# Performance work log

Measured on AMD Instinct MI355X. Metric: run time of the kernel, lower is better.

The kernel has to match this reference:

```python
import jax, jax.numpy as jnp
import numpy as np

B, T, D = 2048, 200, 64
H1, H2 = 80, 40
NEG_INF = -4294967295.0  # -(2**32) + 1 as in original


def setup_inputs() -> dict:
    key0 = jax.random.key(0)
    ks = jax.random.split(key0, 10)
    din_dim = 4 * D
    inp = {
        "query": jax.random.normal(ks[0], (B, D), dtype=jnp.float32),
        "key": jax.random.normal(ks[1], (B, T, D), dtype=jnp.float32),
        "mask": jax.random.randint(ks[2], (B,), 1, T + 1, dtype=jnp.int32),
        # MLP params (Dense 4D->80->40->1, use_bias=True)
        "W1": jax.random.normal(ks[3], (din_dim, H1), dtype=jnp.float32) / np.sqrt(din_dim),
        "b1": jnp.zeros((H1,), dtype=jnp.float32),
        "W2": jax.random.normal(ks[4], (H1, H2), dtype=jnp.float32) / np.sqrt(H1),
        "b2": jnp.zeros((H2,), dtype=jnp.float32),
        "W3": jax.random.normal(ks[5], (H2, 1), dtype=jnp.float32) / np.sqrt(H2),
        "b3": jnp.zeros((1,), dtype=jnp.float32),
    }
    return inp


def reference(query, key, mask, W1, b1, W2, b2, W3, b3):
    b, t, d = key.shape
    q = query[:, None, :]                      # [B,1,D]
    q_tile = jnp.broadcast_to(q, (b, t, d))    # [B,T,D]
    din_all = jnp.concatenate([q_tile, key, q_tile - key, q_tile * key], axis=-1)  # [B,T,4D]
    h = jax.nn.sigmoid(jnp.einsum("btf,fh->bth", din_all, W1) + b1)
    h = jax.nn.sigmoid(jnp.einsum("bth,hg->btg", h, W2) + b2)
    score = (jnp.einsum("btg,go->bto", h, W3) + b3)[..., 0]  # [B,T]
    key_mask = jnp.arange(t)[None, :] < mask[:, None]        # [B,T]
    score = jnp.where(key_mask, score, NEG_INF)
    score = score / jnp.asarray(d, score.dtype) ** 0.5
    attn = jax.nn.softmax(score, axis=-1)                    # [B,T]
    out = jnp.einsum("bt,btd->bd", attn, key)                # [B,D] (squeezed)
    return out
```

## Files before the change

kernel.cpp:

```cpp
#include <hip/hip_runtime.h>
#include <math.h>

#define B_  2048
#define T_  200
#define D_  64
#define H1_ 80
#define H2_ 40

#define VSTR 72
#define WSTR 104
#define HSTR 104

#define WS_A    0
#define WS_C    10240
#define WS_W2T  20480
#define WS_ACT  30464

typedef __bf16 bf16x8 __attribute__((ext_vector_type(8)));
typedef float  f32x4  __attribute__((ext_vector_type(4)));

__device__ __forceinline__ float sigmoidf_(float x) {
    return __builtin_amdgcn_rcpf(1.0f + __expf(-x));
}

__global__ __launch_bounds__(256)
void prep_kernel(const float* __restrict__ W1, const float* __restrict__ W2,
                 void* __restrict__ ws)
{
    __bf16* A    = (__bf16*)((char*)ws + WS_A);
    __bf16* C    = (__bf16*)((char*)ws + WS_C);
    __bf16* W2Tp = (__bf16*)((char*)ws + WS_W2T);
    float*  acT  = (float*)((char*)ws + WS_ACT);
    const int e0 = blockIdx.x * 256 + threadIdx.x;

    for (int e = e0; e < H1_ * D_; e += 2048) {
        int h = e >> 6, f = e & 63;
        float wb = W1[(64  + f) * H1_ + h];
        float wc = W1[(128 + f) * H1_ + h];
        float wd = W1[(192 + f) * H1_ + h];
        float wa = W1[f * H1_ + h];
        A[e]   = (__bf16)(wb - wc);
        C[e]   = (__bf16)wd;
        acT[e] = wa + wc;
    }
    for (int e = e0; e < 48 * WSTR; e += 2048) {
        int g = e / WSTR, h = e - g * WSTR;
        W2Tp[e] = (g < H2_ && h < H1_) ? (__bf16)W2[h * H2_ + g] : (__bf16)0.0f;
    }
}

__global__ __launch_bounds__(256, 2)
void attn_din9(const float* __restrict__ query,
               const float* __restrict__ key,
               const int*   __restrict__ mask,
               const float* __restrict__ b1,
               const float* __restrict__ b2,
               const float* __restrict__ W3,
               const float* __restrict__ b3,
               const void*  __restrict__ ws,
               float* __restrict__ out)
{
    __shared__ __align__(16) __bf16 s_V[4][H1_ * VSTR];
    __shared__ __align__(16) __bf16 s_h1[4][16 * HSTR];
    __shared__ float  s_scf[4][208];
    __shared__ float  s_q[4][D_];
    __shared__ float  s_base[4][H1_];

    const int tid  = threadIdx.x;
    const int lane = tid & 63;
    const int w    = tid >> 6;
    const int c16  = lane & 15;
    const int g16  = lane >> 4;
    const int b    = blockIdx.x * 4 + w;

    const int   mv     = mask[b];
    const int   ntiles = (mv + 15) >> 4;
    const float b3v    = b3[0];
    const float* kb = key + (size_t)b * T_ * D_;

    const __bf16* wsA   = (const __bf16*)((const char*)ws + WS_A);
    const __bf16* wsC   = (const __bf16*)((const char*)ws + WS_C);
    const __bf16* wsW2T = (const __bf16*)((const char*)ws + WS_W2T);
    const float*  wsacT = (const float*) ((const char*)ws + WS_ACT);

    float qv = query[b * D_ + lane];
    float4 u0, u1, u2, u3;
    {
        int tr = c16;
        const float* kr = kb + (size_t)tr * D_ + g16 * 8;
        u0 = *(const float4*)(kr);
        u1 = *(const float4*)(kr + 4);
        u2 = *(const float4*)(kr + 32);
        u3 = *(const float4*)(kr + 36);
    }

    s_scf[w][lane]       = -1e30f;
    s_scf[w][64 + lane]  = -1e30f;
    s_scf[w][128 + lane] = -1e30f;
    if (lane < 16) s_scf[w][192 + lane] = -1e30f;

    bf16x8 bw[3][3];
    #pragma unroll
    for (int nt = 0; nt < 3; ++nt)
        #pragma unroll
        for (int ks = 0; ks < 3; ++ks)
            bw[nt][ks] = *(const bf16x8*)&wsW2T[(nt * 16 + c16) * WSTR + ks * 32 + g16 * 8];

    float b2c[3], w3c[3];
    #pragma unroll
    for (int nt = 0; nt < 3; ++nt) {
        int g = nt * 16 + c16;
        b2c[nt] = (g < H2_) ? b2[g] : 0.0f;
        w3c[nt] = (g < H2_) ? W3[g] : 0.0f;
    }

    s_q[w][lane] = qv;

    #pragma unroll
    for (int i = 0; i < 10; ++i) {
        int e = lane + 64 * i;
        int h = e >> 3, f8 = e & 7;
        bf16x8 a8 = *(const bf16x8*)&wsA[e * 8];
        bf16x8 c8 = *(const bf16x8*)&wsC[e * 8];
        f32x4 q0 = *(const f32x4*)&s_q[w][f8 * 8];
        f32x4 q1 = *(const f32x4*)&s_q[w][f8 * 8 + 4];
        bf16x8 v8;
        v8[0] = (__bf16)((float)a8[0] + q0[0] * (float)c8[0]);
        v8[1] = (__bf16)((float)a8[1] + q0[1] * (float)c8[1]);
        v8[2] = (__bf16)((float)a8[2] + q0[2] * (float)c8[2]);
        v8[3] = (__bf16)((float)a8[3] + q0[3] * (float)c8[3]);
        v8[4] = (__bf16)((float)a8[4] + q1[0] * (float)c8[4]);
        v8[5] = (__bf16)((float)a8[5] + q1[1] * (float)c8[5]);
        v8[6] = (__bf16)((float)a8[6] + q1[2] * (float)c8[6]);
        v8[7] = (__bf16)((float)a8[7] + q1[3] * (float)c8[7]);
        *(bf16x8*)&s_V[w][h * VSTR + f8 * 8] = v8;
    }

    {
        float a0 = b1[lane], a1 = 0.0f, a2 = 0.0f, a3 = 0.0f;
        const f32x4* row = (const f32x4*)&wsacT[lane * D_];
        #pragma unroll
        for (int f4 = 0; f4 < 16; ++f4) {
            f32x4 v  = row[f4];
            f32x4 q4 = *(const f32x4*)&s_q[w][f4 * 4];
            a0 = fmaf(q4[0], v[0], a0);
            a1 = fmaf(q4[1], v[1], a1);
            a2 = fmaf(q4[2], v[2], a2);
            a3 = fmaf(q4[3], v[3], a3);
        }
        s_base[w][lane] = (a0 + a1) + (a2 + a3);
    }
    if (lane < 16) {
        int h = 64 + lane;
        float a0 = b1[h], a1 = 0.0f, a2 = 0.0f, a3 = 0.0f;
        const f32x4* row = (const f32x4*)&wsacT[h * D_];
        #pragma unroll
        for (int f4 = 0; f4 < 16; ++f4) {
            f32x4 v  = row[f4];
            f32x4 q4 = *(const f32x4*)&s_q[w][f4 * 4];
            a0 = fmaf(q4[0], v[0], a0);
            a1 = fmaf(q4[1], v[1], a1);
            a2 = fmaf(q4[2], v[2], a2);
            a3 = fmaf(q4[3], v[3], a3);
        }
        s_base[w][h] = (a0 + a1) + (a2 + a3);
    }

    {
        int row = lane & 15, c0 = 80 + (lane >> 4) * 4;
        *(uint2*)&s_h1[w][row * HSTR + c0] = make_uint2(0u, 0u);
    }

    float base_c[5];
    #pragma unroll
    for (int nt = 0; nt < 5; ++nt) base_c[nt] = s_base[w][nt * 16 + c16];
    __bf16* myh = &s_h1[w][0];

    for (int tt = 0; tt < ntiles; ++tt) {
        bf16x8 af0, af1;
        af0[0] = (__bf16)u0.x; af0[1] = (__bf16)u0.y; af0[2] = (__bf16)u0.z; af0[3] = (__bf16)u0.w;
        af0[4] = (__bf16)u1.x; af0[5] = (__bf16)u1.y; af0[6] = (__bf16)u1.z; af0[7] = (__bf16)u1.w;
        af1[0] = (__bf16)u2.x; af1[1] = (__bf16)u2.y; af1[2] = (__bf16)u2.z; af1[3] = (__bf16)u2.w;
        af1[4] = (__bf16)u3.x; af1[5] = (__bf16)u3.y; af1[6] = (__bf16)u3.z; af1[7] = (__bf16)u3.w;

        if (tt + 1 < ntiles) {
            int tr = (tt + 1) * 16 + c16;
            const float* kr = kb + (size_t)((tr < T_) ? tr : (T_ - 1)) * D_ + g16 * 8;
            u0 = *(const float4*)(kr);
            u1 = *(const float4*)(kr + 4);
            u2 = *(const float4*)(kr + 32);
            u3 = *(const float4*)(kr + 36);
        }

        #pragma unroll
        for (int nt = 0; nt < 5; ++nt) {
            float bb = base_c[nt];
            f32x4 c = { bb, bb, bb, bb };
            bf16x8 bv0 = *(const bf16x8*)&s_V[w][(nt * 16 + c16) * VSTR + g16 * 8];
            bf16x8 bv1 = *(const bf16x8*)&s_V[w][(nt * 16 + c16) * VSTR + 32 + g16 * 8];
            c = __builtin_amdgcn_mfma_f32_16x16x32_bf16(af0, bv0, c, 0, 0, 0);
            c = __builtin_amdgcn_mfma_f32_16x16x32_bf16(af1, bv1, c, 0, 0, 0);
            #pragma unroll
            for (int r = 0; r < 4; ++r)
                myh[(g16 * 4 + r) * HSTR + nt * 16 + c16] = (__bf16)sigmoidf_(c[r]);
        }

        bf16x8 a2_0 = *(const bf16x8*)&myh[c16 * HSTR + g16 * 8];
        bf16x8 a2_1 = *(const bf16x8*)&myh[c16 * HSTR + 32 + g16 * 8];
        bf16x8 a2_2 = *(const bf16x8*)&myh[c16 * HSTR + 64 + g16 * 8];
        f32x4 acc2[3];
        #pragma unroll
        for (int nt = 0; nt < 3; ++nt) {
            float bb = b2c[nt];
            f32x4 c = { bb, bb, bb, bb };
            c = __builtin_amdgcn_mfma_f32_16x16x32_bf16(a2_0, bw[nt][0], c, 0, 0, 0);
            c = __builtin_amdgcn_mfma_f32_16x16x32_bf16(a2_1, bw[nt][1], c, 0, 0, 0);
            c = __builtin_amdgcn_mfma_f32_16x16x32_bf16(a2_2, bw[nt][2], c, 0, 0, 0);
            acc2[nt] = c;
        }

        const int tb = tt * 16;
        #pragma unroll
        for (int r = 0; r < 4; ++r) {
            float partial = sigmoidf_(acc2[0][r]) * w3c[0]
                          + sigmoidf_(acc2[1][r]) * w3c[1]
                          + sigmoidf_(acc2[2][r]) * w3c[2];
            partial += __shfl_xor(partial, 1);
            partial += __shfl_xor(partial, 2);
            partial += __shfl_xor(partial, 4);
            partial += __shfl_xor(partial, 8);
            int t = tb + g16 * 4 + r;
            if (c16 == 0 && t < mv)
                s_scf[w][t] = (partial + b3v) * 0.125f;
        }
    }
    asm volatile("s_waitcnt lgkmcnt(0)" ::: "memory");

    float s0 = s_scf[w][lane];
    float s1 = s_scf[w][64 + lane];
    float s2 = s_scf[w][128 + lane];
    float s3 = (lane < 16) ? s_scf[w][192 + lane] : -1e30f;
    float m = fmaxf(fmaxf(s0, s1), fmaxf(s2, s3));
    #pragma unroll
    for (int off = 32; off >= 1; off >>= 1) m = fmaxf(m, __shfl_xor(m, off));
    float p0 = __expf(s0 - m), p1 = __expf(s1 - m);
    float p2 = __expf(s2 - m), p3 = (lane < 16) ? __expf(s3 - m) : 0.0f;
    float ps = (p0 + p1) + (p2 + p3);
    #pragma unroll
    for (int off = 32; off >= 1; off >>= 1) ps += __shfl_xor(ps, off);
    float inv_total = __builtin_amdgcn_rcpf(ps);
    s_scf[w][lane]       = p0;
    s_scf[w][64 + lane]  = p1;
    s_scf[w][128 + lane] = p2;
    if (lane < 16) s_scf[w][192 + lane] = p3;
    asm volatile("s_waitcnt lgkmcnt(0)" ::: "memory");

    float a0 = 0.0f, a1 = 0.0f, a2s = 0.0f, a3s = 0.0f;
    const float* ksc = &s_scf[w][0];
    int t = 0;
    for (; t + 4 <= mv; t += 4) {
        a0  = fmaf(ksc[t],     kb[(t)     * D_ + lane], a0);
        a1  = fmaf(ksc[t + 1], kb[(t + 1) * D_ + lane], a1);
        a2s = fmaf(ksc[t + 2], kb[(t + 2) * D_ + lane], a2s);
        a3s = fmaf(ksc[t + 3], kb[(t + 3) * D_ + lane], a3s);
    }
    for (; t < mv; ++t)
        a0 = fmaf(ksc[t], kb[t * D_ + lane], a0);
    out[b * D_ + lane] = ((a0 + a1) + (a2s + a3s)) * inv_total;
}

extern "C" void kernel_launch(void* const* d_in, const int* in_sizes, int n_in,
                              void* d_out, int out_size, void* d_ws, size_t ws_size,
                              hipStream_t stream)
{
    const float* query = (const float*)d_in[0];
    const float* key   = (const float*)d_in[1];
    const int*   mask  = (const int*)  d_in[2];
    const float* W1    = (const float*)d_in[3];
    const float* b1    = (const float*)d_in[4];
    const float* W2    = (const float*)d_in[5];
    const float* b2    = (const float*)d_in[6];
    const float* W3    = (const float*)d_in[7];
    const float* b3    = (const float*)d_in[8];
    float* out = (float*)d_out;

    prep_kernel<<<8, 256, 0, stream>>>(W1, W2, d_ws);
    attn_din9<<<512, 256, 0, stream>>>(query, key, mask, b1, b2, W3, b3, d_ws, out);
}
```

Before: 47.49 us.

## Fuse online softmax and weighted key sum into MLP tile loop; keep V in registers

Replaces the post-loop softmax and second pass over the key rows with an online (flash-style) softmax. The loop rescales running max, sum and per-lane output accumulators each 16-row tile, using the key values already loaded for the MFMA A operand. This removes the second global read of key and the score buffer in shared memory. The per-batch first-layer weight matrix V is now built directly in registers as MFMA B fragments instead of staged through LDS. The cost is higher register pressure (extra accumulators plus 10 bf16x8 fragments) and per-tile shuffle reductions.

Result: slower. 49.18 us (+3.6%).

```diff
diff --git a/kernel.cpp b/kernel.cpp
--- a/kernel.cpp
+++ b/kernel.cpp
@@ -7,7 +7,6 @@
 #define H1_ 80
 #define H2_ 40
 
-#define VSTR 72
 #define WSTR 104
 #define HSTR 104
 
@@ -50,21 +49,21 @@
 }
 
 __global__ __launch_bounds__(256, 2)
-void attn_din9(const float* __restrict__ query,
-               const float* __restrict__ key,
-               const int*   __restrict__ mask,
-               const float* __restrict__ b1,
-               const float* __restrict__ b2,
-               const float* __restrict__ W3,
-               const float* __restrict__ b3,
-               const void*  __restrict__ ws,
-               float* __restrict__ out)
+void attn_din10(const float* __restrict__ query,
+                const float* __restrict__ key,
+                const int*   __restrict__ mask,
+                const float* __restrict__ b1,
+                const float* __restrict__ b2,
+                const float* __restrict__ W3,
+                const float* __restrict__ b3,
+                const void*  __restrict__ ws,
+                float* __restrict__ out)
 {
-    __shared__ __align__(16) __bf16 s_V[4][H1_ * VSTR];
     __shared__ __align__(16) __bf16 s_h1[4][16 * HSTR];
-    __shared__ float  s_scf[4][208];
-    __shared__ float  s_q[4][D_];
-    __shared__ float  s_base[4][H1_];
+    __shared__ __align__(16) float  s_q[4][D_];
+    __shared__ float s_base[4][H1_];
+    __shared__ float s_sc16[4][16];
+    __shared__ float s_part[4][D_];
 
     const int tid  = threadIdx.x;
     const int lane = tid & 63;
@@ -86,18 +85,13 @@
     float qv = query[b * D_ + lane];
     float4 u0, u1, u2, u3;
     {
-        int tr = c16;
-        const float* kr = kb + (size_t)tr * D_ + g16 * 8;
+        const float* kr = kb + (size_t)c16 * D_ + g16 * 8;
         u0 = *(const float4*)(kr);
         u1 = *(const float4*)(kr + 4);
         u2 = *(const float4*)(kr + 32);
         u3 = *(const float4*)(kr + 36);
     }
-
-    s_scf[w][lane]       = -1e30f;
-    s_scf[w][64 + lane]  = -1e30f;
-    s_scf[w][128 + lane] = -1e30f;
-    if (lane < 16) s_scf[w][192 + lane] = -1e30f;
+    s_q[w][lane] = qv;
 
     bf16x8 bw[3][3];
     #pragma unroll
@@ -112,28 +106,6 @@
         int g = nt * 16 + c16;
         b2c[nt] = (g < H2_) ? b2[g] : 0.0f;
         w3c[nt] = (g < H2_) ? W3[g] : 0.0f;
-    }
-
-    s_q[w][lane] = qv;
-
-    #pragma unroll
-    for (int i = 0; i < 10; ++i) {
-        int e = lane + 64 * i;
-        int h = e >> 3, f8 = e & 7;
-        bf16x8 a8 = *(const bf16x8*)&wsA[e * 8];
-        bf16x8 c8 = *(const bf16x8*)&wsC[e * 8];
-        f32x4 q0 = *(const f32x4*)&s_q[w][f8 * 8];
-        f32x4 q1 = *(const f32x4*)&s_q[w][f8 * 8 + 4];
-        bf16x8 v8;
-        v8[0] = (__bf16)((float)a8[0] + q0[0] * (float)c8[0]);
-        v8[1] = (__bf16)((float)a8[1] + q0[1] * (float)c8[1]);
-        v8[2] = (__bf16)((float)a8[2] + q0[2] * (float)c8[2]);
-        v8[3] = (__bf16)((float)a8[3] + q0[3] * (float)c8[3]);
-        v8[4] = (__bf16)((float)a8[4] + q1[0] * (float)c8[4]);
-        v8[5] = (__bf16)((float)a8[5] + q1[1] * (float)c8[5]);
-        v8[6] = (__bf16)((float)a8[6] + q1[2] * (float)c8[6]);
-        v8[7] = (__bf16)((float)a8[7] + q1[3] * (float)c8[7]);
-        *(bf16x8*)&s_V[w][h * VSTR + f8 * 8] = v8;
     }
 
     {
@@ -166,6 +138,28 @@
         s_base[w][h] = (a0 + a1) + (a2 + a3);
     }
 
+    bf16x8 bv[5][2];
+    #pragma unroll
+    for (int nt = 0; nt < 5; ++nt)
+        #pragma unroll
+        for (int ks = 0; ks < 2; ++ks) {
+            int off = (nt * 16 + c16) * D_ + ks * 32 + g16 * 8;
+            bf16x8 a8 = *(const bf16x8*)&wsA[off];
+            bf16x8 c8 = *(const bf16x8*)&wsC[off];
+            f32x4 q0 = *(const f32x4*)&s_q[w][ks * 32 + g16 * 8];
+            f32x4 q1 = *(const f32x4*)&s_q[w][ks * 32 + g16 * 8 + 4];
+            bf16x8 v8;
+            v8[0] = (__bf16)((float)a8[0] + q0[0] * (float)c8[0]);
+            v8[1] = (__bf16)((float)a8[1] + q0[1] * (float)c8[1]);
+            v8[2] = (__bf16)((float)a8[2] + q0[2] * (float)c8[2]);
+            v8[3] = (__bf16)((float)a8[3] + q0[3] * (float)c8[3]);
+            v8[4] = (__bf16)((float)a8[4] + q1[0] * (float)c8[4]);
+            v8[5] = (__bf16)((float)a8[5] + q1[1] * (float)c8[5]);
+            v8[6] = (__bf16)((float)a8[6] + q1[2] * (float)c8[6]);
+            v8[7] = (__bf16)((float)a8[7] + q1[3] * (float)c8[7]);
+            bv[nt][ks] = v8;
+        }
+
     {
         int row = lane & 15, c0 = 80 + (lane >> 4) * 4;
         *(uint2*)&s_h1[w][row * HSTR + c0] = make_uint2(0u, 0u);
@@ -175,6 +169,10 @@
     #pragma unroll
     for (int nt = 0; nt < 5; ++nt) base_c[nt] = s_base[w][nt * 16 + c16];
     __bf16* myh = &s_h1[w][0];
+
+    float o00,o01,o02,o03,o04,o05,o06,o07,o08,o09,o10,o11,o12,o13,o14,o15;
+    o00=o01=o02=o03=o04=o05=o06=o07=o08=o09=o10=o11=o12=o13=o14=o15=0.0f;
+    float m_run = -1e30f, l_run = 0.0f;
 
     for (int tt = 0; tt < ntiles; ++tt) {
         bf16x8 af0, af1;
@@ -183,23 +181,22 @@
         af1[0] = (__bf16)u2.x; af1[1] = (__bf16)u2.y; af1[2] = (__bf16)u2.z; af1[3] = (__bf16)u2.w;
         af1[4] = (__bf16)u3.x; af1[5] = (__bf16)u3.y; af1[6] = (__bf16)u3.z; af1[7] = (__bf16)u3.w;
 
+        float4 n0 = u0, n1 = u1, n2 = u2, n3 = u3;
         if (tt + 1 < ntiles) {
             int tr = (tt + 1) * 16 + c16;
             const float* kr = kb + (size_t)((tr < T_) ? tr : (T_ - 1)) * D_ + g16 * 8;
-            u0 = *(const float4*)(kr);
-            u1 = *(const float4*)(kr + 4);
-            u2 = *(const float4*)(kr + 32);
-            u3 = *(const float4*)(kr + 36);
+            n0 = *(const float4*)(kr);
+            n1 = *(const float4*)(kr + 4);
+            n2 = *(const float4*)(kr + 32);
+            n3 = *(const float4*)(kr + 36);
         }
 
         #pragma unroll
         for (int nt = 0; nt < 5; ++nt) {
             float bb = base_c[nt];
             f32x4 c = { bb, bb, bb, bb };
-            bf16x8 bv0 = *(const bf16x8*)&s_V[w][(nt * 16 + c16) * VSTR + g16 * 8];
-            bf16x8 bv1 = *(const bf16x8*)&s_V[w][(nt * 16 + c16) * VSTR + 32 + g16 * 8];
-            c = __builtin_amdgcn_mfma_f32_16x16x32_bf16(af0, bv0, c, 0, 0, 0);
-            c = __builtin_amdgcn_mfma_f32_16x16x32_bf16(af1, bv1, c, 0, 0, 0);
+            c = __builtin_amdgcn_mfma_f32_16x16x32_bf16(af0, bv[nt][0], c, 0, 0, 0);
+            c = __builtin_amdgcn_mfma_f32_16x16x32_bf16(af1, bv[nt][1], c, 0, 0, 0);
             #pragma unroll
             for (int r = 0; r < 4; ++r)
                 myh[(g16 * 4 + r) * HSTR + nt * 16 + c16] = (__bf16)sigmoidf_(c[r]);
@@ -229,44 +226,58 @@
             partial += __shfl_xor(partial, 2);
             partial += __shfl_xor(partial, 4);
             partial += __shfl_xor(partial, 8);
-            int t = tb + g16 * 4 + r;
-            if (c16 == 0 && t < mv)
-                s_scf[w][t] = (partial + b3v) * 0.125f;
-        }
+            if (c16 == 0) {
+                int t = tb + g16 * 4 + r;
+                s_sc16[w][g16 * 4 + r] = (t < mv) ? (partial + b3v) * 0.125f : -1e30f;
+            }
+        }
+
+        float s = s_sc16[w][c16];
+        float tm = s;
+        tm = fmaxf(tm, __shfl_xor(tm, 1));
+        tm = fmaxf(tm, __shfl_xor(tm, 2));
+        tm = fmaxf(tm, __shfl_xor(tm, 4));
+        tm = fmaxf(tm, __shfl_xor(tm, 8));
+        float m_new = fmaxf(m_run, tm);
+        float alpha = __expf(m_run - m_new);
+        float p = __expf(s - m_new);
+        float psum = p;
+        psum += __shfl_xor(psum, 1);
+        psum += __shfl_xor(psum, 2);
+        psum += __shfl_xor(psum, 4);
+        psum += __shfl_xor(psum, 8);
+        l_run = l_run * alpha + psum;
+        o00 = o00 * alpha + p * u0.x;  o01 = o01 * alpha + p * u0.y;
+        o02 = o02 * alpha + p * u0.z;  o03 = o03 * alpha + p * u0.w;
+        o04 = o04 * alpha + p * u1.x;  o05 = o05 * alpha + p * u1.y;
+        o06 = o06 * alpha + p * u1.z;  o07 = o07 * alpha + p * u1.w;
+        o08 = o08 * alpha + p * u2.x;  o09 = o09 * alpha + p * u2.y;
+        o10 = o10 * alpha + p * u2.z;  o11 = o11 * alpha + p * u2.w;
+        o12 = o12 * alpha + p * u3.x;  o13 = o13 * alpha + p * u3.y;
+        o14 = o14 * alpha + p * u3.z;  o15 = o15 * alpha + p * u3.w;
+        m_run = m_new;
+
+        u0 = n0; u1 = n1; u2 = n2; u3 = n3;
+    }
+
+    #define ORED(X) X += __shfl_xor(X,1); X += __shfl_xor(X,2); X += __shfl_xor(X,4); X += __shfl_xor(X,8);
+    ORED(o00) ORED(o01) ORED(o02) ORED(o03) ORED(o04) ORED(o05) ORED(o06) ORED(o07)
+    ORED(o08) ORED(o09) ORED(o10) ORED(o11) ORED(o12) ORED(o13) ORED(o14) ORED(o15)
+    #undef ORED
+    float inv_total = __builtin_amdgcn_rcpf(l_run);
+    if (c16 == 0) {
+        float* sp = &s_part[w][0];
+        sp[g16 * 8 + 0] = o00;  sp[g16 * 8 + 1] = o01;
+        sp[g16 * 8 + 2] = o02;  sp[g16 * 8 + 3] = o03;
+        sp[g16 * 8 + 4] = o04;  sp[g16 * 8 + 5] = o05;
+        sp[g16 * 8 + 6] = o06;  sp[g16 * 8 + 7] = o07;
+        sp[32 + g16 * 8 + 0] = o08;  sp[32 + g16 * 8 + 1] = o09;
+        sp[32 + g16 * 8 + 2] = o10;  sp[32 + g16 * 8 + 3] = o11;
+        sp[32 + g16 * 8 + 4] = o12;  sp[32 + g16 * 8 + 5] = o13;
+        sp[32 + g16 * 8 + 6] = o14;  sp[32 + g16 * 8 + 7] = o15;
     }
     asm volatile("s_waitcnt lgkmcnt(0)" ::: "memory");
-
-    float s0 = s_scf[w][lane];
-    float s1 = s_scf[w][64 + lane];
-    float s2 = s_scf[w][128 + lane];
-    float s3 = (lane < 16) ? s_scf[w][192 + lane] : -1e30f;
-    float m = fmaxf(fmaxf(s0, s1), fmaxf(s2, s3));
-    #pragma unroll
-    for (int off = 32; off >= 1; off >>= 1) m = fmaxf(m, __shfl_xor(m, off));
-    float p0 = __expf(s0 - m), p1 = __expf(s1 - m);
-    float p2 = __expf(s2 - m), p3 = (lane < 16) ? __expf(s3 - m) : 0.0f;
-    float ps = (p0 + p1) + (p2 + p3);
-    #pragma unroll
-    for (int off = 32; off >= 1; off >>= 1) ps += __shfl_xor(ps, off);
-    float inv_total = __builtin_amdgcn_rcpf(ps);
-    s_scf[w][lane]       = p0;
-    s_scf[w][64 + lane]  = p1;
-    s_scf[w][128 + lane] = p2;
-    if (lane < 16) s_scf[w][192 + lane] = p3;
-    asm volatile("s_waitcnt lgkmcnt(0)" ::: "memory");
-
-    float a0 = 0.0f, a1 = 0.0f, a2s = 0.0f, a3s = 0.0f;
-    const float* ksc = &s_scf[w][0];
-    int t = 0;
-    for (; t + 4 <= mv; t += 4) {
-        a0  = fmaf(ksc[t],     kb[(t)     * D_ + lane], a0);
-        a1  = fmaf(ksc[t + 1], kb[(t + 1) * D_ + lane], a1);
-        a2s = fmaf(ksc[t + 2], kb[(t + 2) * D_ + lane], a2s);
-        a3s = fmaf(ksc[t + 3], kb[(t + 3) * D_ + lane], a3s);
-    }
-    for (; t < mv; ++t)
-        a0 = fmaf(ksc[t], kb[t * D_ + lane], a0);
-    out[b * D_ + lane] = ((a0 + a1) + (a2s + a3s)) * inv_total;
+    out[b * D_ + lane] = s_part[w][lane] * inv_total;
 }
 
 extern "C" void kernel_launch(void* const* d_in, const int* in_sizes, int n_in,
@@ -285,5 +296,5 @@
     float* out = (float*)d_out;
 
     prep_kernel<<<8, 256, 0, stream>>>(W1, W2, d_ws);
-    attn_din9<<<512, 256, 0, stream>>>(query, key, mask, b1, b2, W3, b3, d_ws, out);
+    attn_din10<<<512, 256, 0, stream>>>(query, key, mask, b1, b2, W3, b3, d_ws, out);
 }
```

## Split each batch row across two waves instead of one wave per row

Applied to the files above, without the earlier changes.

Each block now handles a single batch row with two waves. The waves interleave the 16-row key tiles and share one s_V/s_base table that is built cooperatively. Softmax max/sum and the final weighted sum are combined across the two waves through shared memory and __syncthreads. This is meant to fix load imbalance from variable mask lengths and halve per-row latency, at the cost of extra block barriers and 2048 smaller blocks.

After: 51.63 us. +8.7%, slower.

```diff
diff --git a/kernel.cpp b/kernel.cpp
--- a/kernel.cpp
+++ b/kernel.cpp
@@ -49,29 +49,31 @@
     }
 }
 
-__global__ __launch_bounds__(256, 2)
-void attn_din9(const float* __restrict__ query,
-               const float* __restrict__ key,
-               const int*   __restrict__ mask,
-               const float* __restrict__ b1,
-               const float* __restrict__ b2,
-               const float* __restrict__ W3,
-               const float* __restrict__ b3,
-               const void*  __restrict__ ws,
-               float* __restrict__ out)
+__global__ __launch_bounds__(128, 3)
+void attn_din12(const float* __restrict__ query,
+                const float* __restrict__ key,
+                const int*   __restrict__ mask,
+                const float* __restrict__ b1,
+                const float* __restrict__ b2,
+                const float* __restrict__ W3,
+                const float* __restrict__ b3,
+                const void*  __restrict__ ws,
+                float* __restrict__ out)
 {
-    __shared__ __align__(16) __bf16 s_V[4][H1_ * VSTR];
-    __shared__ __align__(16) __bf16 s_h1[4][16 * HSTR];
-    __shared__ float  s_scf[4][208];
-    __shared__ float  s_q[4][D_];
-    __shared__ float  s_base[4][H1_];
+    __shared__ __align__(16) __bf16 s_V[H1_ * VSTR];
+    __shared__ __align__(16) __bf16 s_h1[2][16 * HSTR];
+    __shared__ float s_scf[208];
+    __shared__ float s_q[D_];
+    __shared__ float s_base[H1_];
+    __shared__ float s_part[2][D_];
+    __shared__ float s_red[4];
 
     const int tid  = threadIdx.x;
     const int lane = tid & 63;
     const int w    = tid >> 6;
     const int c16  = lane & 15;
     const int g16  = lane >> 4;
-    const int b    = blockIdx.x * 4 + w;
+    const int b    = blockIdx.x;
 
     const int   mv     = mask[b];
     const int   ntiles = (mv + 15) >> 4;
@@ -83,21 +85,8 @@
     const __bf16* wsW2T = (const __bf16*)((const char*)ws + WS_W2T);
     const float*  wsacT = (const float*) ((const char*)ws + WS_ACT);
 
-    float qv = query[b * D_ + lane];
-    float4 u0, u1, u2, u3;
-    {
-        int tr = c16;
-        const float* kr = kb + (size_t)tr * D_ + g16 * 8;
-        u0 = *(const float4*)(kr);
-        u1 = *(const float4*)(kr + 4);
-        u2 = *(const float4*)(kr + 32);
-        u3 = *(const float4*)(kr + 36);
-    }
-
-    s_scf[w][lane]       = -1e30f;
-    s_scf[w][64 + lane]  = -1e30f;
-    s_scf[w][128 + lane] = -1e30f;
-    if (lane < 16) s_scf[w][192 + lane] = -1e30f;
+    if (w == 0) s_q[lane] = query[b * D_ + lane];
+    for (int i = tid; i < 208; i += 128) s_scf[i] = -1e30f;
 
     bf16x8 bw[3][3];
     #pragma unroll
@@ -113,17 +102,16 @@
         b2c[nt] = (g < H2_) ? b2[g] : 0.0f;
         w3c[nt] = (g < H2_) ? W3[g] : 0.0f;
     }
-
-    s_q[w][lane] = qv;
-
-    #pragma unroll
-    for (int i = 0; i < 10; ++i) {
-        int e = lane + 64 * i;
+    __syncthreads();
+
+    #pragma unroll
+    for (int i = 0; i < 5; ++i) {
+        int e = tid + 128 * i;
         int h = e >> 3, f8 = e & 7;
         bf16x8 a8 = *(const bf16x8*)&wsA[e * 8];
         bf16x8 c8 = *(const bf16x8*)&wsC[e * 8];
-        f32x4 q0 = *(const f32x4*)&s_q[w][f8 * 8];
-        f32x4 q1 = *(const f32x4*)&s_q[w][f8 * 8 + 4];
+        f32x4 q0 = *(const f32x4*)&s_q[f8 * 8];
+        f32x4 q1 = *(const f32x4*)&s_q[f8 * 8 + 4];
         bf16x8 v8;
         v8[0] = (__bf16)((float)a8[0] + q0[0] * (float)c8[0]);
         v8[1] = (__bf16)((float)a8[1] + q0[1] * (float)c8[1]);
@@ -133,58 +121,54 @@
         v8[5] = (__bf16)((float)a8[5] + q1[1] * (float)c8[5]);
         v8[6] = (__bf16)((float)a8[6] + q1[2] * (float)c8[6]);
         v8[7] = (__bf16)((float)a8[7] + q1[3] * (float)c8[7]);
-        *(bf16x8*)&s_V[w][h * VSTR + f8 * 8] = v8;
-    }
-
-    {
-        float a0 = b1[lane], a1 = 0.0f, a2 = 0.0f, a3 = 0.0f;
-        const f32x4* row = (const f32x4*)&wsacT[lane * D_];
+        *(bf16x8*)&s_V[h * VSTR + f8 * 8] = v8;
+    }
+
+    if (tid < H1_) {
+        float a0 = b1[tid], a1 = 0.0f, a2 = 0.0f, a3 = 0.0f;
+        const f32x4* row = (const f32x4*)&wsacT[tid * D_];
         #pragma unroll
         for (int f4 = 0; f4 < 16; ++f4) {
             f32x4 v  = row[f4];
-            f32x4 q4 = *(const f32x4*)&s_q[w][f4 * 4];
+            f32x4 q4 = *(const f32x4*)&s_q[f4 * 4];
             a0 = fmaf(q4[0], v[0], a0);
             a1 = fmaf(q4[1], v[1], a1);
             a2 = fmaf(q4[2], v[2], a2);
             a3 = fmaf(q4[3], v[3], a3);
         }
-        s_base[w][lane] = (a0 + a1) + (a2 + a3);
-    }
-    if (lane < 16) {
-        int h = 64 + lane;
-        float a0 = b1[h], a1 = 0.0f, a2 = 0.0f, a3 = 0.0f;
-        const f32x4* row = (const f32x4*)&wsacT[h * D_];
-        #pragma unroll
-        for (int f4 = 0; f4 < 16; ++f4) {
-            f32x4 v  = row[f4];
-            f32x4 q4 = *(const f32x4*)&s_q[w][f4 * 4];
-            a0 = fmaf(q4[0], v[0], a0);
-            a1 = fmaf(q4[1], v[1], a1);
-            a2 = fmaf(q4[2], v[2], a2);
-            a3 = fmaf(q4[3], v[3], a3);
-        }
-        s_base[w][h] = (a0 + a1) + (a2 + a3);
+        s_base[tid] = (a0 + a1) + (a2 + a3);
     }
 
     {
         int row = lane & 15, c0 = 80 + (lane >> 4) * 4;
         *(uint2*)&s_h1[w][row * HSTR + c0] = make_uint2(0u, 0u);
     }
+    __syncthreads();
 
     float base_c[5];
     #pragma unroll
-    for (int nt = 0; nt < 5; ++nt) base_c[nt] = s_base[w][nt * 16 + c16];
+    for (int nt = 0; nt < 5; ++nt) base_c[nt] = s_base[nt * 16 + c16];
     __bf16* myh = &s_h1[w][0];
 
-    for (int tt = 0; tt < ntiles; ++tt) {
+    float4 u0, u1, u2, u3;
+    {
+        int tr = w * 16 + c16;
+        const float* kr = kb + (size_t)((tr < T_) ? tr : (T_ - 1)) * D_ + g16 * 8;
+        u0 = *(const float4*)(kr);
+        u1 = *(const float4*)(kr + 4);
+        u2 = *(const float4*)(kr + 32);
+        u3 = *(const float4*)(kr + 36);
+    }
+
+    for (int tt = w; tt < ntiles; tt += 2) {
         bf16x8 af0, af1;
         af0[0] = (__bf16)u0.x; af0[1] = (__bf16)u0.y; af0[2] = (__bf16)u0.z; af0[3] = (__bf16)u0.w;
         af0[4] = (__bf16)u1.x; af0[5] = (__bf16)u1.y; af0[6] = (__bf16)u1.z; af0[7] = (__bf16)u1.w;
         af1[0] = (__bf16)u2.x; af1[1] = (__bf16)u2.y; af1[2] = (__bf16)u2.z; af1[3] = (__bf16)u2.w;
         af1[4] = (__bf16)u3.x; af1[5] = (__bf16)u3.y; af1[6] = (__bf16)u3.z; af1[7] = (__bf16)u3.w;
 
-        if (tt + 1 < ntiles) {
-            int tr = (tt + 1) * 16 + c16;
+        if (tt + 2 < ntiles) {
+            int tr = (tt + 2) * 16 + c16;
             const float* kr = kb + (size_t)((tr < T_) ? tr : (T_ - 1)) * D_ + g16 * 8;
             u0 = *(const float4*)(kr);
             u1 = *(const float4*)(kr + 4);
@@ -196,8 +180,8 @@
         for (int nt = 0; nt < 5; ++nt) {
             float bb = base_c[nt];
             f32x4 c = { bb, bb, bb, bb };
-            bf16x8 bv0 = *(const bf16x8*)&s_V[w][(nt * 16 + c16) * VSTR + g16 * 8];
-            bf16x8 bv1 = *(const bf16x8*)&s_V[w][(nt * 16 + c16) * VSTR + 32 + g16 * 8];
+            bf16x8 bv0 = *(const bf16x8*)&s_V[(nt * 16 + c16) * VSTR + g16 * 8];
+            bf16x8 bv1 = *(const bf16x8*)&s_V[(nt * 16 + c16) * VSTR + 32 + g16 * 8];
             c = __builtin_amdgcn_mfma_f32_16x16x32_bf16(af0, bv0, c, 0, 0, 0);
             c = __builtin_amdgcn_mfma_f32_16x16x32_bf16(af1, bv1, c, 0, 0, 0);
             #pragma unroll
@@ -231,42 +215,49 @@
             partial += __shfl_xor(partial, 8);
             int t = tb + g16 * 4 + r;
             if (c16 == 0 && t < mv)
-                s_scf[w][t] = (partial + b3v) * 0.125f;
-        }
-    }
-    asm volatile("s_waitcnt lgkmcnt(0)" ::: "memory");
-
-    float s0 = s_scf[w][lane];
-    float s1 = s_scf[w][64 + lane];
-    float s2 = s_scf[w][128 + lane];
-    float s3 = (lane < 16) ? s_scf[w][192 + lane] : -1e30f;
-    float m = fmaxf(fmaxf(s0, s1), fmaxf(s2, s3));
+                s_scf[t] = (partial + b3v) * 0.125f;
+        }
+    }
+    __syncthreads();
+
+    float s0 = s_scf[tid];
+    float s1 = (tid + 128 < 208) ? s_scf[tid + 128] : -1e30f;
+    float m = fmaxf(s0, s1);
     #pragma unroll
     for (int off = 32; off >= 1; off >>= 1) m = fmaxf(m, __shfl_xor(m, off));
-    float p0 = __expf(s0 - m), p1 = __expf(s1 - m);
-    float p2 = __expf(s2 - m), p3 = (lane < 16) ? __expf(s3 - m) : 0.0f;
-    float ps = (p0 + p1) + (p2 + p3);
+    if (lane == 0) s_red[w] = m;
+    __syncthreads();
+    m = fmaxf(s_red[0], s_red[1]);
+    float p0 = __expf(s0 - m);
+    float p1 = (tid + 128 < 208) ? __expf(s1 - m) : 0.0f;
+    float ps = p0 + p1;
     #pragma unroll
     for (int off = 32; off >= 1; off >>= 1) ps += __shfl_xor(ps, off);
-    float inv_total = __builtin_amdgcn_rcpf(ps);
-    s_scf[w][lane]       = p0;
-    s_scf[w][64 + lane]  = p1;
-    s_scf[w][128 + lane] = p2;
-    if (lane < 16) s_scf[w][192 + lane] = p3;
-    asm volatile("s_waitcnt lgkmcnt(0)" ::: "memory");
+    if (lane == 0) s_red[2 + w] = ps;
+    __syncthreads();
+    float inv_total = __builtin_amdgcn_rcpf(s_red[2] + s_red[3]);
+    s_scf[tid] = p0;
+    if (tid + 128 < 208) s_scf[tid + 128] = p1;
+    __syncthreads();
 
     float a0 = 0.0f, a1 = 0.0f, a2s = 0.0f, a3s = 0.0f;
-    const float* ksc = &s_scf[w][0];
-    int t = 0;
-    for (; t + 4 <= mv; t += 4) {
-        a0  = fmaf(ksc[t],     kb[(t)     * D_ + lane], a0);
-        a1  = fmaf(ksc[t + 1], kb[(t + 1) * D_ + lane], a1);
-        a2s = fmaf(ksc[t + 2], kb[(t + 2) * D_ + lane], a2s);
-        a3s = fmaf(ksc[t + 3], kb[(t + 3) * D_ + lane], a3s);
-    }
-    for (; t < mv; ++t)
-        a0 = fmaf(ksc[t], kb[t * D_ + lane], a0);
-    out[b * D_ + lane] = ((a0 + a1) + (a2s + a3s)) * inv_total;
+    for (int tt = w; tt < ntiles; tt += 2) {
+        int t0 = tt * 16;
+        int tend = (t0 + 16 < mv) ? (t0 + 16) : mv;
+        int t = t0;
+        for (; t + 4 <= tend; t += 4) {
+            a0  = fmaf(s_scf[t],     kb[(t)     * D_ + lane], a0);
+            a1  = fmaf(s_scf[t + 1], kb[(t + 1) * D_ + lane], a1);
+            a2s = fmaf(s_scf[t + 2], kb[(t + 2) * D_ + lane], a2s);
+            a3s = fmaf(s_scf[t + 3], kb[(t + 3) * D_ + lane], a3s);
+        }
+        for (; t < tend; ++t)
+            a0 = fmaf(s_scf[t], kb[t * D_ + lane], a0);
+    }
+    s_part[w][lane] = (a0 + a1) + (a2s + a3s);
+    __syncthreads();
+    if (tid < D_)
+        out[b * D_ + tid] = (s_part[0][tid] + s_part[1][tid]) * inv_total;
 }
 
 extern "C" void kernel_launch(void* const* d_in, const int* in_sizes, int n_in,
@@ -285,5 +276,5 @@
     float* out = (float*)d_out;
 
     prep_kernel<<<8, 256, 0, stream>>>(W1, W2, d_ws);
-    attn_din9<<<512, 256, 0, stream>>>(query, key, mask, b1, b2, W3, b3, d_ws, out);
-}
+    attn_din12<<<B_, 128, 0, stream>>>(query, key, mask, b1, b2, W3, b3, d_ws, out);
+}
```
